# Kernel optimization log

Hardware: AMD Instinct MI355X
Metric: run time of the kernel (lower is better)

## Reference

```python
import jax, jax.numpy as jnp
import numpy as np
from jax import lax

EPS = 1e-8

def setup_inputs() -> dict:
    key = jax.random.key(0)
    k1, k2, k3, k4 = jax.random.split(key, 4)
    b, ic, oc, ks, sd, h, w = 16, 512, 512, 3, 512, 64, 64
    x = jax.random.normal(k1, (b, ic, h, w), dtype=jnp.float32)
    style = jax.random.normal(k2, (b, sd), dtype=jnp.float32)
    # kaiming_normal_(fan_in, linear): std = 1/sqrt(ic*ks*ks)
    weight = jax.random.normal(k3, (oc, ic, ks, ks), dtype=jnp.float32) / np.sqrt(ic * ks * ks)
    bias = jnp.zeros((oc,), dtype=jnp.float32)
    # nn.Linear default init ~ U(-1/sqrt(sd), 1/sqrt(sd)); normal approx is fine for a baseline
    mod_w = jax.random.normal(k4, (ic, sd), dtype=jnp.float32) / np.sqrt(sd)
    mod_b = jnp.ones((ic,), dtype=jnp.float32)  # bias initialized to 1.0 in the module
    return {"x": x, "style": style, "weight": weight, "bias": bias, "mod_w": mod_w, "mod_b": mod_b}

def reference(x, style, weight, bias, mod_w, mod_b):
    b, ic, h, w = x.shape
    oc, _, ks, _ = weight.shape
    # style modulation: [b, ic]
    s = style @ mod_w.T + mod_b
    # per-sample modulated weights: [b, oc, ic, k, k]
    wmod = weight[None] * s[:, None, :, None, None]
    # demodulation
    demod = lax.rsqrt(jnp.sum(wmod * wmod, axis=(2, 3, 4)) + EPS)  # [b, oc]
    wmod = wmod * demod[:, :, None, None, None]
    pad = ks // 2
    # grouped conv with groups=b == per-sample conv: vmap over batch
    def conv1(xi, wi):  # xi: [ic,h,w], wi: [oc,ic,k,k]
        return lax.conv_general_dilated(
            xi[None], wi, window_strides=(1, 1),
            padding=[(pad, pad), (pad, pad)],
            dimension_numbers=("NCHW", "OIHW", "NCHW"))[0]
    out = jax.vmap(conv1)(x, wmod)  # [b, oc, h, w]
    return out + bias[None, :, None, None]
```

## Files before the change

### kernel.cpp

```cpp
#include <hip/hip_runtime.h>
#include <hip/hip_bf16.h>


typedef __bf16 bf16x8 __attribute__((ext_vector_type(8)));
typedef float  f32x4  __attribute__((ext_vector_type(4)));

#define IC   512
#define OC   512
#define HW   4096
#define KTOT 4608

typedef __attribute__((address_space(3))) unsigned lds_u32;
typedef const __attribute__((address_space(1))) unsigned glb_u32;
#define GLL16(gsrc, ldst) \
    __builtin_amdgcn_global_load_lds((glb_u32*)(gsrc), (lds_u32*)(ldst), 16, 0, 0)
#define VMW(N)  asm volatile("s_waitcnt vmcnt(" #N ")" ::: "memory")
#define BAR()   asm volatile("s_barrier" ::: "memory")
#define SCHED0() __builtin_amdgcn_sched_barrier(0)

__global__ __launch_bounds__(256) void style_mod_kernel(
    const float* __restrict__ style, const float* __restrict__ mod_w,
    const float* __restrict__ mod_b, float* __restrict__ s_out)
{
    int pair = blockIdx.x * 4 + (threadIdx.x >> 6);
    int lane = threadIdx.x & 63;
    int b = pair >> 9;
    int i = pair & 511;
    const float4* sv = (const float4*)(style + b * 512);
    const float4* wv = (const float4*)(mod_w + i * 512);
    float4 a0 = sv[lane * 2], a1 = sv[lane * 2 + 1];
    float4 w0 = wv[lane * 2], w1 = wv[lane * 2 + 1];
    float sum = a0.x*w0.x + a0.y*w0.y + a0.z*w0.z + a0.w*w0.w
              + a1.x*w1.x + a1.y*w1.y + a1.z*w1.z + a1.w*w1.w;
    #pragma unroll
    for (int off = 32; off; off >>= 1) sum += __shfl_xor(sum, off);
    if (lane == 0) s_out[pair] = sum + mod_b[i];
}

__global__ __launch_bounds__(256) void wmod_kernel(
    const float* __restrict__ weight,
    const float* __restrict__ s_in,
    __hip_bfloat16* __restrict__ wmod)
{
    int oc = blockIdx.x;
    __shared__ float w_sh[4608];
    __shared__ float s_sh[8192];
    __shared__ float q_sh[512];
    __shared__ float demod_sh[16];
    int t = threadIdx.x;
    const float* wrow = weight + (size_t)oc * KTOT;
    for (int e = t; e < 4608; e += 256) w_sh[e] = wrow[e];
    for (int e = t; e < 8192; e += 256) s_sh[e] = s_in[e];
    __syncthreads();
    for (int ic = t; ic < 512; ic += 256) {
        float q = 0.f;
        #pragma unroll
        for (int tap = 0; tap < 9; ++tap) { float w = w_sh[ic * 9 + tap]; q += w * w; }
        q_sh[ic] = q;
    }
    __syncthreads();
    int bb = t >> 4, li = t & 15;
    float part = 0.f;
    for (int ic = li; ic < 512; ic += 16) {
        float sv = s_sh[bb * 512 + ic];
        part += q_sh[ic] * sv * sv;
    }
    #pragma unroll
    for (int off = 8; off; off >>= 1) part += __shfl_xor(part, off, 16);
    if (li == 0) demod_sh[bb] = rsqrtf(part + 1e-8f);
    __syncthreads();
    for (int b2 = 0; b2 < 16; ++b2) {
        float dm = demod_sh[b2];
        const float* srow = s_sh + b2 * 512;
        __hip_bfloat16* dst = wmod + ((size_t)b2 * 512 + oc) * KTOT;
        for (int ep = t; ep < 4608; ep += 256) {
            int tap = ep >> 9, ic = ep & 511;
            dst[ep] = __float2bfloat16(w_sh[ic * 9 + tap] * srow[ic] * dm);
        }
    }
}

__global__ void zero_row_kernel(__hip_bfloat16* xT) {
    ((unsigned*)(xT + ((size_t)blockIdx.x * 4097 + 4096) * 512))[threadIdx.x] = 0u;
}

__global__ __launch_bounds__(256) void xpose_kernel(
    const float* __restrict__ x, __hip_bfloat16* __restrict__ xT)
{
    __shared__ __align__(16) float tile[64][68];
    int b = blockIdx.z, ic0 = blockIdx.y * 64, p0 = blockIdx.x * 64;
    int t = threadIdx.x;
    const float* xb = x + ((size_t)b * 512 + ic0) * 4096 + p0;
    int rr = t >> 4, cc = (t & 15) * 4;
    #pragma unroll
    for (int i = 0; i < 4; ++i) {
        float4 v = *(const float4*)(xb + (size_t)(rr + i * 16) * 4096 + cc);
        *(float4*)&tile[rr + i * 16][cc] = v;
    }
    __syncthreads();
    int pr = t >> 2, io = (t & 3) * 16;
    __hip_bfloat16 obuf[16];
    #pragma unroll
    for (int j = 0; j < 16; ++j) obuf[j] = __float2bfloat16(tile[io + j][pr]);
    __hip_bfloat16* dst = xT + ((size_t)b * 4097 + p0 + pr) * 512 + ic0 + io;
    *(uint4*)dst       = *(uint4*)&obuf[0];
    *(uint4*)(dst + 8) = *(uint4*)&obuf[8];
}

__global__ __launch_bounds__(512, 2) void conv_kernel(
    const __hip_bfloat16* __restrict__ xT,
    const __hip_bfloat16* __restrict__ wmod,
    const float* __restrict__ bias,
    float* __restrict__ out)
{
    __shared__ __align__(16) __hip_bfloat16 Ash[4][256 * 32];
    __shared__ __align__(16) __hip_bfloat16 Bsh[4][256 * 32];

    const int t    = threadIdx.x;
    const int lane = t & 63;
    const int wid  = t >> 6;
    const int wm   = wid >> 2;
    const int wn   = wid & 3;
    const int lr   = lane & 15;
    const int lq   = lane >> 4;

    int bid = blockIdx.x;
    int xcd = bid & 7, idx = bid >> 3;
    int oc1 = idx & 1;
    int nt  = (idx >> 1) & 15;
    int bb  = (idx >> 5) & 1;
    int b   = xcd * 2 + bb;
    int oc0 = oc1 * 256, n0 = nt * 256;

    const __hip_bfloat16* wb = wmod + (size_t)(b * 512 + oc0) * KTOT;
    const __hip_bfloat16* xb = xT + (size_t)b * 4097 * 512;

    const int qoff = (((t & 3) ^ ((t >> 3) & 3)) * 8);
    const int srow = t >> 2;
    const int p0g  = n0 + srow;
    const int y0p  = p0g >> 6, x0p = p0g & 63;

    const __hip_bfloat16* pA0 = wb + (size_t)srow * KTOT + qoff;
    const __hip_bfloat16* pA1 = pA0 + (size_t)128 * KTOT;

    const int swq = (lq ^ ((lr >> 1) & 3)) * 8;
    const int arb = (wm * 128 + lr) * 32 + swq;
    const int brb = (wn * 64  + lr) * 32 + swq;

    f32x4 acc[8][4] = {};

    auto bptrs = [&](int tap, const __hip_bfloat16*& P0, const __hip_bfloat16*& P1) {
        int dy = tap / 3 - 1, dx = tap % 3 - 1;
        int sy = y0p + dy, sx = x0p + dx;
        int pix0 = ((((unsigned)sy)  < 64u) & (((unsigned)sx) < 64u)) ? ((sy  << 6) + sx) : 4096;
        int sy1 = sy + 2;
        int pix1 = ((((unsigned)sy1) < 64u) & (((unsigned)sx) < 64u)) ? ((sy1 << 6) + sx) : 4096;
        P0 = xb + (size_t)pix0 * 512 + qoff;
        P1 = xb + (size_t)pix1 * 512 + qoff;
    };

#define STAGE_A(SB, OFF) { \
    GLL16(pA0 + (OFF), &Ash[SB][t * 8]); \
    GLL16(pA1 + (OFF), &Ash[SB][(t + 512) * 8]); }
#define STAGE_B(SB, Q0, Q1, OFF) { \
    GLL16((Q0) + (OFF), &Bsh[SB][t * 8]); \
    GLL16((Q1) + (OFF), &Bsh[SB][(t + 512) * 8]); }

#define MFMA_HALF(MB) { \
    __builtin_amdgcn_s_setprio(1); \
    _Pragma("unroll") for (int mi = 0; mi < 4; ++mi) \
        _Pragma("unroll") for (int ni = 0; ni < 4; ++ni) \
            acc[(MB) + mi][ni] = __builtin_amdgcn_mfma_f32_16x16x32_bf16( \
                af[mi], bfr[ni], acc[(MB) + mi][ni], 0, 0, 0); \
    __builtin_amdgcn_s_setprio(0); }

    const __hip_bfloat16 *pB0, *pB1, *nB0, *nB1;
    bptrs(0, pB0, pB1);

    STAGE_A(0, 0);  STAGE_B(0, pB0, pB1, 0);
    STAGE_A(1, 32); STAGE_B(1, pB0, pB1, 32);
    STAGE_A(2, 64); STAGE_B(2, pB0, pB1, 64);
    VMW(8);
    BAR();

    for (int tap = 0; tap < 8; ++tap) {
        bptrs(tap + 1, nB0, nB1);
        #pragma unroll
        for (int ch = 0; ch < 16; ++ch) {
            const int cb = ch & 3, sb = (ch + 3) & 3;
            bf16x8 af[4], bfr[4];
            #pragma unroll
            for (int mi = 0; mi < 4; ++mi)
                af[mi] = *(const bf16x8*)(&Ash[cb][arb + mi * 512]);
            #pragma unroll
            for (int ni = 0; ni < 4; ++ni)
                bfr[ni] = *(const bf16x8*)(&Bsh[cb][brb + ni * 512]);
            STAGE_A(sb, (ch + 3) * 32);
            BAR(); SCHED0();
            MFMA_HALF(0);
            BAR();
            #pragma unroll
            for (int mi = 0; mi < 4; ++mi)
                af[mi] = *(const bf16x8*)(&Ash[cb][arb + (4 + mi) * 512]);
            if (ch < 13) { STAGE_B(sb, pB0, pB1, (ch + 3) * 32); }
            else         { STAGE_B(sb, nB0, nB1, (ch - 13) * 32); }
            BAR(); SCHED0();
            MFMA_HALF(4);
            VMW(8);
            BAR();
        }
        pA0 += 512; pA1 += 512;
        pB0 = nB0; pB1 = nB1;
    }
    #pragma unroll
    for (int ch = 0; ch < 16; ++ch) {
        const int cb = ch & 3, sb = (ch + 3) & 3;
        bf16x8 af[4], bfr[4];
        #pragma unroll
        for (int mi = 0; mi < 4; ++mi)
            af[mi] = *(const bf16x8*)(&Ash[cb][arb + mi * 512]);
        #pragma unroll
        for (int ni = 0; ni < 4; ++ni)
            bfr[ni] = *(const bf16x8*)(&Bsh[cb][brb + ni * 512]);
        if (ch <= 12) STAGE_A(sb, (ch + 3) * 32);
        BAR(); SCHED0();
        MFMA_HALF(0);
        BAR();
        #pragma unroll
        for (int mi = 0; mi < 4; ++mi)
            af[mi] = *(const bf16x8*)(&Ash[cb][arb + (4 + mi) * 512]);
        if (ch <= 12) STAGE_B(sb, pB0, pB1, (ch + 3) * 32);
        BAR(); SCHED0();
        MFMA_HALF(4);
        if      (ch < 13)  { VMW(8); BAR(); }
        else if (ch == 13) { VMW(4); BAR(); }
        else if (ch == 14) { VMW(0); BAR(); }
    }
#undef STAGE_A
#undef STAGE_B
#undef MFMA_HALF

    #pragma unroll
    for (int mi = 0; mi < 8; ++mi) {
        int oc = oc0 + wm * 128 + mi * 16 + lq * 4;
        #pragma unroll
        for (int ni = 0; ni < 4; ++ni) {
            int n = n0 + wn * 64 + ni * 16 + lr;
            #pragma unroll
            for (int v = 0; v < 4; ++v) {
                float r = acc[mi][ni][v] + bias[oc + v];
                out[((size_t)(b * OC + oc + v)) * HW + n] = r;
            }
        }
    }
}

extern "C" void kernel_launch(void* const* d_in, const int* in_sizes, int n_in,
                              void* d_out, int out_size, void* d_ws, size_t ws_size,
                              hipStream_t stream) {
    const float* x      = (const float*)d_in[0];
    const float* style  = (const float*)d_in[1];
    const float* weight = (const float*)d_in[2];
    const float* bias   = (const float*)d_in[3];
    const float* mod_w  = (const float*)d_in[4];
    const float* mod_b  = (const float*)d_in[5];
    float* out = (float*)d_out;

    float* s_ws = (float*)d_ws;
    __hip_bfloat16* wmod = (__hip_bfloat16*)((char*)d_ws + 32768);
    __hip_bfloat16* xT   = (__hip_bfloat16*)((char*)d_ws + 32768 + (size_t)16 * 512 * KTOT * 2);

    style_mod_kernel<<<2048, 256, 0, stream>>>(style, mod_w, mod_b, s_ws);
    wmod_kernel<<<512, 256, 0, stream>>>(weight, s_ws, wmod);
    zero_row_kernel<<<16, 256, 0, stream>>>(xT);
    dim3 tgrid(64, 8, 16);
    xpose_kernel<<<tgrid, 256, 0, stream>>>(x, xT);
    conv_kernel<<<512, 512, 0, stream>>>(xT, wmod, bias, out);
}
```

Before: 339.0 us.

## Software-pipeline LDS fragment loads with register double buffering, one barrier per step

```diff
diff --git a/kernel.cpp b/kernel.cpp
--- a/kernel.cpp
+++ b/kernel.cpp
@@ -14,9 +14,13 @@
 typedef const __attribute__((address_space(1))) unsigned glb_u32;
 #define GLL16(gsrc, ldst) \
     __builtin_amdgcn_global_load_lds((glb_u32*)(gsrc), (lds_u32*)(ldst), 16, 0, 0)
-#define VMW(N)  asm volatile("s_waitcnt vmcnt(" #N ")" ::: "memory")
 #define BAR()   asm volatile("s_barrier" ::: "memory")
-#define SCHED0() __builtin_amdgcn_sched_barrier(0)
+
+template<int N> __device__ __forceinline__ void vmw() {
+    asm volatile("s_waitcnt vmcnt(%0)" :: "n"(N) : "memory");
+}
+
+#define MFMA1(A, B, C) __builtin_amdgcn_mfma_f32_16x16x32_bf16(A, B, C, 0, 0, 0)
 
 __global__ __launch_bounds__(256) void style_mod_kernel(
     const float* __restrict__ style, const float* __restrict__ mod_w,
@@ -148,6 +152,7 @@
     const int brb = (wn * 64  + lr) * 32 + swq;
 
     f32x4 acc[8][4] = {};
+    bf16x8 aL[2][4], bR[2][4];
 
     auto bptrs = [&](int tap, const __hip_bfloat16*& P0, const __hip_bfloat16*& P1) {
         int dy = tap / 3 - 1, dx = tap % 3 - 1;
@@ -166,13 +171,42 @@
     GLL16((Q0) + (OFF), &Bsh[SB][t * 8]); \
     GLL16((Q1) + (OFF), &Bsh[SB][(t + 512) * 8]); }
 
-#define MFMA_HALF(MB) { \
+#define STEP(CH, DO_STAGE, DO_PF, NQ0, NQ1, VN, DO_VMW) { \
+    const int cs = (CH) & 3, ps = ((CH) + 1) & 3, ss = ((CH) + 3) & 3; \
+    const int cp = (CH) & 1, np = ((CH) + 1) & 1; \
+    bf16x8 ah0 = *(const bf16x8*)(&Ash[cs][arb + 2048]); \
+    bf16x8 ah1 = *(const bf16x8*)(&Ash[cs][arb + 2560]); \
+    bf16x8 ah2 = *(const bf16x8*)(&Ash[cs][arb + 3072]); \
+    bf16x8 ah3 = *(const bf16x8*)(&Ash[cs][arb + 3584]); \
+    if (DO_STAGE) { \
+        STAGE_A(ss, ((CH) + 3) * 32); \
+        if ((CH) < 13) { STAGE_B(ss, pB0, pB1, ((CH) + 3) * 32); } \
+        else           { STAGE_B(ss, NQ0, NQ1, ((CH) - 13) * 32); } \
+    } \
     __builtin_amdgcn_s_setprio(1); \
-    _Pragma("unroll") for (int mi = 0; mi < 4; ++mi) \
+    _Pragma("unroll") for (int ni = 0; ni < 4; ++ni) { \
+        acc[0][ni] = MFMA1(aL[cp][0], bR[cp][ni], acc[0][ni]); \
+        acc[1][ni] = MFMA1(aL[cp][1], bR[cp][ni], acc[1][ni]); \
+        acc[2][ni] = MFMA1(aL[cp][2], bR[cp][ni], acc[2][ni]); \
+        acc[3][ni] = MFMA1(aL[cp][3], bR[cp][ni], acc[3][ni]); \
+    } \
+    __builtin_amdgcn_s_setprio(0); \
+    if (DO_PF) { \
+        _Pragma("unroll") for (int mi = 0; mi < 4; ++mi) \
+            aL[np][mi] = *(const bf16x8*)(&Ash[ps][arb + mi * 512]); \
         _Pragma("unroll") for (int ni = 0; ni < 4; ++ni) \
-            acc[(MB) + mi][ni] = __builtin_amdgcn_mfma_f32_16x16x32_bf16( \
-                af[mi], bfr[ni], acc[(MB) + mi][ni], 0, 0, 0); \
-    __builtin_amdgcn_s_setprio(0); }
+            bR[np][ni] = *(const bf16x8*)(&Bsh[ps][brb + ni * 512]); \
+    } \
+    __builtin_amdgcn_s_setprio(1); \
+    _Pragma("unroll") for (int ni = 0; ni < 4; ++ni) { \
+        acc[4][ni] = MFMA1(ah0, bR[cp][ni], acc[4][ni]); \
+        acc[5][ni] = MFMA1(ah1, bR[cp][ni], acc[5][ni]); \
+        acc[6][ni] = MFMA1(ah2, bR[cp][ni], acc[6][ni]); \
+        acc[7][ni] = MFMA1(ah3, bR[cp][ni], acc[7][ni]); \
+    } \
+    __builtin_amdgcn_s_setprio(0); \
+    if (DO_VMW) { vmw<VN>(); } \
+    BAR(); }
 
     const __hip_bfloat16 *pB0, *pB1, *nB0, *nB1;
     bptrs(0, pB0, pB1);
@@ -180,65 +214,51 @@
     STAGE_A(0, 0);  STAGE_B(0, pB0, pB1, 0);
     STAGE_A(1, 32); STAGE_B(1, pB0, pB1, 32);
     STAGE_A(2, 64); STAGE_B(2, pB0, pB1, 64);
-    VMW(8);
+    vmw<4>();
     BAR();
+    #pragma unroll
+    for (int mi = 0; mi < 4; ++mi)
+        aL[0][mi] = *(const bf16x8*)(&Ash[0][arb + mi * 512]);
+    #pragma unroll
+    for (int ni = 0; ni < 4; ++ni)
+        bR[0][ni] = *(const bf16x8*)(&Bsh[0][brb + ni * 512]);
 
     for (int tap = 0; tap < 8; ++tap) {
         bptrs(tap + 1, nB0, nB1);
         #pragma unroll
         for (int ch = 0; ch < 16; ++ch) {
-            const int cb = ch & 3, sb = (ch + 3) & 3;
-            bf16x8 af[4], bfr[4];
-            #pragma unroll
-            for (int mi = 0; mi < 4; ++mi)
-                af[mi] = *(const bf16x8*)(&Ash[cb][arb + mi * 512]);
-            #pragma unroll
-            for (int ni = 0; ni < 4; ++ni)
-                bfr[ni] = *(const bf16x8*)(&Bsh[cb][brb + ni * 512]);
-            STAGE_A(sb, (ch + 3) * 32);
-            BAR(); SCHED0();
-            MFMA_HALF(0);
-            BAR();
-            #pragma unroll
-            for (int mi = 0; mi < 4; ++mi)
-                af[mi] = *(const bf16x8*)(&Ash[cb][arb + (4 + mi) * 512]);
-            if (ch < 13) { STAGE_B(sb, pB0, pB1, (ch + 3) * 32); }
-            else         { STAGE_B(sb, nB0, nB1, (ch - 13) * 32); }
-            BAR(); SCHED0();
-            MFMA_HALF(4);
-            VMW(8);
-            BAR();
+            STEP(ch, true, true, nB0, nB1, 4, true);
         }
         pA0 += 512; pA1 += 512;
         pB0 = nB0; pB1 = nB1;
     }
-    #pragma unroll
-    for (int ch = 0; ch < 16; ++ch) {
-        const int cb = ch & 3, sb = (ch + 3) & 3;
-        bf16x8 af[4], bfr[4];
-        #pragma unroll
-        for (int mi = 0; mi < 4; ++mi)
-            af[mi] = *(const bf16x8*)(&Ash[cb][arb + mi * 512]);
-        #pragma unroll
-        for (int ni = 0; ni < 4; ++ni)
-            bfr[ni] = *(const bf16x8*)(&Bsh[cb][brb + ni * 512]);
-        if (ch <= 12) STAGE_A(sb, (ch + 3) * 32);
-        BAR(); SCHED0();
-        MFMA_HALF(0);
-        BAR();
-        #pragma unroll
-        for (int mi = 0; mi < 4; ++mi)
-            af[mi] = *(const bf16x8*)(&Ash[cb][arb + (4 + mi) * 512]);
-        if (ch <= 12) STAGE_B(sb, pB0, pB1, (ch + 3) * 32);
-        BAR(); SCHED0();
-        MFMA_HALF(4);
-        if      (ch < 13)  { VMW(8); BAR(); }
-        else if (ch == 13) { VMW(4); BAR(); }
-        else if (ch == 14) { VMW(0); BAR(); }
-    }
+
+    #pragma unroll
+    for (int ch = 0; ch < 13; ++ch) {
+        STEP(ch, true, true, nB0, nB1, 4, true);
+    }
+    STEP(13, false, true, nB0, nB1, 0, true);
+    STEP(14, false, true, nB0, nB1, 0, false);
+    {
+        bf16x8 ah0 = *(const bf16x8*)(&Ash[3][arb + 2048]);
+        bf16x8 ah1 = *(const bf16x8*)(&Ash[3][arb + 2560]);
+        bf16x8 ah2 = *(const bf16x8*)(&Ash[3][arb + 3072]);
+        bf16x8 ah3 = *(const bf16x8*)(&Ash[3][arb + 3584]);
+        #pragma unroll
+        for (int ni = 0; ni < 4; ++ni) {
+            acc[0][ni] = MFMA1(aL[1][0], bR[1][ni], acc[0][ni]);
+            acc[1][ni] = MFMA1(aL[1][1], bR[1][ni], acc[1][ni]);
+            acc[2][ni] = MFMA1(aL[1][2], bR[1][ni], acc[2][ni]);
+            acc[3][ni] = MFMA1(aL[1][3], bR[1][ni], acc[3][ni]);
+            acc[4][ni] = MFMA1(ah0, bR[1][ni], acc[4][ni]);
+            acc[5][ni] = MFMA1(ah1, bR[1][ni], acc[5][ni]);
+            acc[6][ni] = MFMA1(ah2, bR[1][ni], acc[6][ni]);
+            acc[7][ni] = MFMA1(ah3, bR[1][ni], acc[7][ni]);
+        }
+    }
+#undef STEP
 #undef STAGE_A
 #undef STAGE_B
-#undef MFMA_HALF
 
     #pragma unroll
     for (int mi = 0; mi < 8; ++mi) {
```

Result: slower. 358.8 us (+5.9%).

## Load A weight fragments directly into registers and drop A LDS staging

Applied to the files above, without the earlier changes.

```diff
diff --git a/kernel.cpp b/kernel.cpp
--- a/kernel.cpp
+++ b/kernel.cpp
@@ -14,9 +14,13 @@
 typedef const __attribute__((address_space(1))) unsigned glb_u32;
 #define GLL16(gsrc, ldst) \
     __builtin_amdgcn_global_load_lds((glb_u32*)(gsrc), (lds_u32*)(ldst), 16, 0, 0)
-#define VMW(N)  asm volatile("s_waitcnt vmcnt(" #N ")" ::: "memory")
 #define BAR()   asm volatile("s_barrier" ::: "memory")
-#define SCHED0() __builtin_amdgcn_sched_barrier(0)
+
+template<int N> __device__ __forceinline__ void vmw() {
+    asm volatile("s_waitcnt vmcnt(%0)" :: "n"(N) : "memory");
+}
+
+#define MFMA1(A, B, C) __builtin_amdgcn_mfma_f32_16x16x32_bf16(A, B, C, 0, 0, 0)
 
 __global__ __launch_bounds__(256) void style_mod_kernel(
     const float* __restrict__ style, const float* __restrict__ mod_w,
@@ -113,7 +117,6 @@
     const float* __restrict__ bias,
     float* __restrict__ out)
 {
-    __shared__ __align__(16) __hip_bfloat16 Ash[4][256 * 32];
     __shared__ __align__(16) __hip_bfloat16 Bsh[4][256 * 32];
 
     const int t    = threadIdx.x;
@@ -140,15 +143,18 @@
     const int p0g  = n0 + srow;
     const int y0p  = p0g >> 6, x0p = p0g & 63;
 
-    const __hip_bfloat16* pA0 = wb + (size_t)srow * KTOT + qoff;
-    const __hip_bfloat16* pA1 = pA0 + (size_t)128 * KTOT;
+    const __hip_bfloat16* pAf[8];
+    #pragma unroll
+    for (int mi = 0; mi < 8; ++mi)
+        pAf[mi] = wb + (size_t)(wm * 128 + mi * 16 + lr) * KTOT + lq * 8;
 
     const int swq = (lq ^ ((lr >> 1) & 3)) * 8;
-    const int arb = (wm * 128 + lr) * 32 + swq;
-    const int brb = (wn * 64  + lr) * 32 + swq;
+    const int brb = (wn * 64 + lr) * 32 + swq;
 
     f32x4 acc[8][4] = {};
-
+    bf16x8 aP[2][8];
+
+    const __hip_bfloat16 *pB0, *pB1, *nB0, *nB1;
     auto bptrs = [&](int tap, const __hip_bfloat16*& P0, const __hip_bfloat16*& P1) {
         int dy = tap / 3 - 1, dx = tap % 3 - 1;
         int sy = y0p + dy, sx = x0p + dx;
@@ -159,86 +165,70 @@
         P1 = xb + (size_t)pix1 * 512 + qoff;
     };
 
-#define STAGE_A(SB, OFF) { \
-    GLL16(pA0 + (OFF), &Ash[SB][t * 8]); \
-    GLL16(pA1 + (OFF), &Ash[SB][(t + 512) * 8]); }
 #define STAGE_B(SB, Q0, Q1, OFF) { \
     GLL16((Q0) + (OFF), &Bsh[SB][t * 8]); \
     GLL16((Q1) + (OFF), &Bsh[SB][(t + 512) * 8]); }
 
-#define MFMA_HALF(MB) { \
-    __builtin_amdgcn_s_setprio(1); \
-    _Pragma("unroll") for (int mi = 0; mi < 4; ++mi) \
+#define STEP(CH, VN, DO_VMW, DO_A, DO_B, BQ0, BQ1, BOFF, DO_BAR) { \
+    if (DO_VMW) { vmw<VN>(); } \
+    if (DO_A) { \
+        _Pragma("unroll") for (int mi = 0; mi < 8; ++mi) \
+            aP[((CH) + 1) & 1][mi] = *(const bf16x8*)(pAf[mi] + ((CH) + 1) * 32); \
+    } \
+    if (DO_B) { STAGE_B(((CH) + 3) & 3, BQ0, BQ1, BOFF); } \
+    { \
+        bf16x8 bv[4]; \
         _Pragma("unroll") for (int ni = 0; ni < 4; ++ni) \
-            acc[(MB) + mi][ni] = __builtin_amdgcn_mfma_f32_16x16x32_bf16( \
-                af[mi], bfr[ni], acc[(MB) + mi][ni], 0, 0, 0); \
-    __builtin_amdgcn_s_setprio(0); }
-
-    const __hip_bfloat16 *pB0, *pB1, *nB0, *nB1;
+            bv[ni] = *(const bf16x8*)(&Bsh[(CH) & 3][brb + ni * 512]); \
+        __builtin_amdgcn_s_setprio(1); \
+        _Pragma("unroll") for (int mi = 0; mi < 8; ++mi) \
+            _Pragma("unroll") for (int ni = 0; ni < 4; ++ni) \
+                acc[mi][ni] = MFMA1(aP[(CH) & 1][mi], bv[ni], acc[mi][ni]); \
+        __builtin_amdgcn_s_setprio(0); \
+    } \
+    if (DO_BAR) { BAR(); } }
+
     bptrs(0, pB0, pB1);
-
-    STAGE_A(0, 0);  STAGE_B(0, pB0, pB1, 0);
-    STAGE_A(1, 32); STAGE_B(1, pB0, pB1, 32);
-    STAGE_A(2, 64); STAGE_B(2, pB0, pB1, 64);
-    VMW(8);
+    STAGE_B(0, pB0, pB1, 0);
+    STAGE_B(1, pB0, pB1, 32);
+    STAGE_B(2, pB0, pB1, 64);
+    #pragma unroll
+    for (int mi = 0; mi < 8; ++mi)
+        aP[0][mi] = *(const bf16x8*)(pAf[mi]);
+    vmw<12>();
     BAR();
 
-    for (int tap = 0; tap < 8; ++tap) {
-        bptrs(tap + 1, nB0, nB1);
-        #pragma unroll
-        for (int ch = 0; ch < 16; ++ch) {
-            const int cb = ch & 3, sb = (ch + 3) & 3;
-            bf16x8 af[4], bfr[4];
+    for (int tap = 0; tap < 9; ++tap) {
+        const bool last = (tap == 8);
+        if (!last) bptrs(tap + 1, nB0, nB1);
+        STEP(0,  2, true, true, true, pB0, pB1,  3 * 32, true);
+        STEP(1,  2, true, true, true, pB0, pB1,  4 * 32, true);
+        STEP(2,  2, true, true, true, pB0, pB1,  5 * 32, true);
+        STEP(3,  2, true, true, true, pB0, pB1,  6 * 32, true);
+        STEP(4,  2, true, true, true, pB0, pB1,  7 * 32, true);
+        STEP(5,  2, true, true, true, pB0, pB1,  8 * 32, true);
+        STEP(6,  2, true, true, true, pB0, pB1,  9 * 32, true);
+        STEP(7,  2, true, true, true, pB0, pB1, 10 * 32, true);
+        STEP(8,  2, true, true, true, pB0, pB1, 11 * 32, true);
+        STEP(9,  2, true, true, true, pB0, pB1, 12 * 32, true);
+        STEP(10, 2, true, true, true, pB0, pB1, 13 * 32, true);
+        STEP(11, 2, true, true, true, pB0, pB1, 14 * 32, true);
+        STEP(12, 2, true, true, true, pB0, pB1, 15 * 32, true);
+        if (!last) {
+            STEP(13, 2, true, true, true, nB0, nB1,  0, true);
+            STEP(14, 2, true, true, true, nB0, nB1, 32, true);
+            STEP(15, 2, true, true, true, nB0, nB1, 64, true);
             #pragma unroll
-            for (int mi = 0; mi < 4; ++mi)
-                af[mi] = *(const bf16x8*)(&Ash[cb][arb + mi * 512]);
-            #pragma unroll
-            for (int ni = 0; ni < 4; ++ni)
-                bfr[ni] = *(const bf16x8*)(&Bsh[cb][brb + ni * 512]);
-            STAGE_A(sb, (ch + 3) * 32);
-            BAR(); SCHED0();
-            MFMA_HALF(0);
-            BAR();
-            #pragma unroll
-            for (int mi = 0; mi < 4; ++mi)
-                af[mi] = *(const bf16x8*)(&Ash[cb][arb + (4 + mi) * 512]);
-            if (ch < 13) { STAGE_B(sb, pB0, pB1, (ch + 3) * 32); }
-            else         { STAGE_B(sb, nB0, nB1, (ch - 13) * 32); }
-            BAR(); SCHED0();
-            MFMA_HALF(4);
-            VMW(8);
-            BAR();
+            for (int mi = 0; mi < 8; ++mi) pAf[mi] += 512;
+            pB0 = nB0; pB1 = nB1;
+        } else {
+            STEP(13, 2, true, true, false, pB0, pB1, 0, true);
+            STEP(14, 0, true, true, false, pB0, pB1, 0, true);
+            STEP(15, 0, false, false, false, pB0, pB1, 0, false);
         }
-        pA0 += 512; pA1 += 512;
-        pB0 = nB0; pB1 = nB1;
-    }
-    #pragma unroll
-    for (int ch = 0; ch < 16; ++ch) {
-        const int cb = ch & 3, sb = (ch + 3) & 3;
-        bf16x8 af[4], bfr[4];
-        #pragma unroll
-        for (int mi = 0; mi < 4; ++mi)
-            af[mi] = *(const bf16x8*)(&Ash[cb][arb + mi * 512]);
-        #pragma unroll
-        for (int ni = 0; ni < 4; ++ni)
-            bfr[ni] = *(const bf16x8*)(&Bsh[cb][brb + ni * 512]);
-        if (ch <= 12) STAGE_A(sb, (ch + 3) * 32);
-        BAR(); SCHED0();
-        MFMA_HALF(0);
-        BAR();
-        #pragma unroll
-        for (int mi = 0; mi < 4; ++mi)
-            af[mi] = *(const bf16x8*)(&Ash[cb][arb + (4 + mi) * 512]);
-        if (ch <= 12) STAGE_B(sb, pB0, pB1, (ch + 3) * 32);
-        BAR(); SCHED0();
-        MFMA_HALF(4);
-        if      (ch < 13)  { VMW(8); BAR(); }
-        else if (ch == 13) { VMW(4); BAR(); }
-        else if (ch == 14) { VMW(0); BAR(); }
-    }
-#undef STAGE_A
+    }
+#undef STEP
 #undef STAGE_B
-#undef MFMA_HALF
 
     #pragma unroll
     for (int mi = 0; mi < 8; ++mi) {
```

After: 1.348 ms. 3.98x slower.
